# Kernel tuning notes

Hardware: AMD Instinct MI355X
Metric: run time of the kernel (lower is better)

The kernel has to match this reference:

```python
import jax, jax.numpy as jnp
import numpy as np

N_HEAD = 8
NORM_GROUPS = 32
EPS = 1e-6


def setup_inputs() -> dict:
    key = jax.random.key(0)
    ks = jax.random.split(key, 9)
    B, C, H, W, D = 1, 256, 16, 16, 16
    COND = 512
    x = jax.random.normal(ks[0], (B, C, H, W, D), dtype=jnp.float32)
    cond = jax.random.normal(ks[1], (B, COND), dtype=jnp.float32)
    # AdaGN linear scale/shift (torch Linear: weight [C, cond_dim], bias [C])
    w_scale = jax.random.normal(ks[2], (C, COND), dtype=jnp.float32) * 0.02
    b_scale = jax.random.normal(ks[3], (C,), dtype=jnp.float32) * 0.02
    w_shift = jax.random.normal(ks[4], (C, COND), dtype=jnp.float32) * 0.02
    b_shift = jax.random.normal(ks[5], (C,), dtype=jnp.float32) * 0.02
    # 1x1x1 conv3d weights collapse to matrices: qkv [3C, C] (no bias), out [C, C] + bias
    w_qkv = jax.random.normal(ks[6], (3 * C, C), dtype=jnp.float32) * (1.0 / np.sqrt(C))
    w_out = jax.random.normal(ks[7], (C, C), dtype=jnp.float32) * (1.0 / np.sqrt(C))
    b_out = jax.random.normal(ks[8], (C,), dtype=jnp.float32) * 0.02
    return {"x": x, "cond": cond, "w_scale": w_scale, "b_scale": b_scale,
            "w_shift": w_shift, "b_shift": b_shift, "w_qkv": w_qkv,
            "w_out": w_out, "b_out": b_out}


def _ada_gn(x, cond, w_scale, b_scale, w_shift, b_shift):
    B, C, H, W, D = x.shape
    G = NORM_GROUPS
    xg = x.reshape(B, G, C // G, H, W, D)
    mean = jnp.mean(xg, axis=(2, 3, 4, 5), keepdims=True)
    var = jnp.var(xg, axis=(2, 3, 4, 5), keepdims=True)
    x_norm = ((xg - mean) * jax.lax.rsqrt(var + EPS)).reshape(B, C, H, W, D)
    scale = (cond @ w_scale.T + b_scale)[:, :, None, None, None]  # [B,C,1,1,1]
    shift = (cond @ w_shift.T + b_shift)[:, :, None, None, None]
    return x_norm * (1.0 + scale) + shift


def reference(x, cond, w_scale, b_scale, w_shift, b_shift, w_qkv, w_out, b_out):
    B, C, H, W, D = x.shape
    nh = N_HEAD
    hd = C // nh
    N = H * W * D  # flattened spatial tokens
    norm = _ada_gn(x, cond, w_scale, b_scale, w_shift, b_shift)
    # 1x1x1 conv == channel matmul
    qkv = jnp.einsum('oc,bchwd->bohwd', w_qkv, norm)        # [B,3C,H,W,D]
    qkv = qkv.reshape(B, nh, 3 * hd, N)
    q, k, v = jnp.split(qkv, 3, axis=2)                      # each [B,nh,hd,N]
    attn = jnp.einsum('bnci,bncj->bnij', q, k) / jnp.sqrt(jnp.float32(C))
    attn = jax.nn.softmax(attn, axis=-1)                     # [B,nh,N,N]
    out = jnp.einsum('bnij,bncj->bnci', attn, v)             # [B,nh,hd,N]
    out = out.reshape(B, C, H, W, D)
    out = jnp.einsum('oc,bchwd->bohwd', w_out, out) + b_out[None, :, None, None, None]
    return out + x
```

## Files before the change

kernel.cpp:

```cpp
#include <hip/hip_runtime.h>
#include <math.h>

#define CCH 256
#define NN  4096
#define NHEAD 8
#define CONDD 512

typedef __attribute__((ext_vector_type(8))) short short8;
typedef __attribute__((ext_vector_type(4))) float f32x4;
typedef __attribute__((ext_vector_type(16))) float f32x16;

static __device__ __forceinline__ short f2bf(float f) {
    union { float f; uint32_t u; } v; v.f = f;
    uint32_t r = v.u + 0x7fffu + ((v.u >> 16) & 1u);
    return (short)(r >> 16);
}

static __device__ __forceinline__ uint32_t cvt_pk_bf16(float a, float b) {
    uint32_t r;
    asm("v_cvt_pk_bf16_f32 %0, %1, %2" : "=v"(r) : "v"(a), "v"(b));
    return r;
}

__global__ __launch_bounds__(256) void front_fused(const float* __restrict__ x,
                                                   const float* __restrict__ cond,
                                                   const float* __restrict__ w_scale,
                                                   const float* __restrict__ b_scale,
                                                   const float* __restrict__ w_shift,
                                                   const float* __restrict__ b_shift,
                                                   const float* __restrict__ wq,
                                                   const float* __restrict__ wo,
                                                   float* __restrict__ partial,
                                                   float* __restrict__ scale,
                                                   float* __restrict__ shift,
                                                   short* __restrict__ wqb,
                                                   short* __restrict__ wob) {
    __shared__ float rs[4], rss[4];
    int bb = blockIdx.x;
    int t = threadIdx.x;
    if (bb < 256) {
        const float4* p = (const float4*)(x + bb * 4096);
        float s = 0.f, ss = 0.f;
        for (int k = t; k < 1024; k += 256) {
            float4 v = p[k];
            s += v.x + v.y + v.z + v.w;
            ss += v.x * v.x + v.y * v.y + v.z * v.z + v.w * v.w;
        }
        #pragma unroll
        for (int off = 32; off; off >>= 1) { s += __shfl_xor(s, off); ss += __shfl_xor(ss, off); }
        int wid = t >> 6;
        if ((t & 63) == 0) { rs[wid] = s; rss[wid] = ss; }
        __syncthreads();
        if (t == 0) {
            partial[2 * bb] = rs[0] + rs[1] + rs[2] + rs[3];
            partial[2 * bb + 1] = rss[0] + rss[1] + rss[2] + rss[3];
        }
    } else if (bb < 1280) {
        int idx = (bb - 256) * 256 + t;
        if (idx < 196608) wqb[idx] = f2bf(wq[idx]);
        else              wob[idx - 196608] = f2bf(wo[idx - 196608]);
    } else {
        int o = (bb - 1280) * 4 + (t >> 6);
        int lane = t & 63;
        float ds = 0.f, dh = 0.f;
        for (int k = lane; k < CONDD; k += 64) {
            float cv = cond[k];
            ds += cv * w_scale[o * CONDD + k];
            dh += cv * w_shift[o * CONDD + k];
        }
        #pragma unroll
        for (int off = 32; off; off >>= 1) { ds += __shfl_xor(ds, off); dh += __shfl_xor(dh, off); }
        if (lane == 0) { scale[o] = ds + b_scale[o]; shift[o] = dh + b_shift[o]; }
    }
}

__global__ __launch_bounds__(256) void normalize_t(const float* __restrict__ x,
                                                   const float* __restrict__ partial,
                                                   const float* __restrict__ scale,
                                                   const float* __restrict__ shift,
                                                   short* __restrict__ norm_t) {
    __shared__ float gm[8], gr[8];
    __shared__ float Aa[64], Bb[64];
    __shared__ short tile[32 * 66];
    int i0 = blockIdx.x * 32;
    int c0 = blockIdx.y * 64;
    int g0 = c0 >> 3;
    int t = threadIdx.x;
    if (t < 8) {
        float s = 0.f, ss = 0.f;
        #pragma unroll
        for (int ch = 0; ch < 8; ++ch) {
            s += partial[((g0 + t) * 8 + ch) * 2];
            ss += partial[((g0 + t) * 8 + ch) * 2 + 1];
        }
        float mean = s * (1.0f / 32768.0f);
        float var = ss * (1.0f / 32768.0f) - mean * mean;
        gm[t] = mean;
        gr[t] = rsqrtf(var + 1e-6f);
    }
    __syncthreads();
    if (t < 64) {
        int c = c0 + t;
        float a = gr[t >> 3] * (1.0f + scale[c]);
        Aa[t] = a;
        Bb[t] = shift[c] - gm[t >> 3] * a;
    }
    __syncthreads();
    #pragma unroll
    for (int e0 = 0; e0 < 8; ++e0) {
        int e = e0 * 256 + t;
        int cl = e >> 5, il = e & 31;
        float v = x[(c0 + cl) * NN + i0 + il];
        tile[il * 66 + cl] = f2bf(v * Aa[cl] + Bb[cl]);
    }
    __syncthreads();
    #pragma unroll
    for (int e0 = 0; e0 < 4; ++e0) {
        int e = e0 * 256 + t;
        int il = e >> 5, cd = e & 31;
        uint32_t d = *(const uint32_t*)&tile[il * 66 + 2 * cd];
        *(uint32_t*)&norm_t[(i0 + il) * 256 + c0 + 2 * cd] = d;
    }
}

__global__ __launch_bounds__(256) void qkv_gemm(const short* __restrict__ wqb,
                                                const short* __restrict__ norm_t,
                                                short* __restrict__ qtb, short* __restrict__ ktb,
                                                short* __restrict__ vcb) {
    int t = threadIdx.x;
    int w = t >> 6, lane = t & 63, li = lane & 15, lg = lane >> 4;
    int o0 = blockIdx.x * 32;
    int i0 = blockIdx.y * 64 + w * 16;
    f32x4 acc[2] = {{0,0,0,0},{0,0,0,0}};
    const short* bbase = norm_t + (i0 + li) * 256 + 8 * lg;
    const short* abase = wqb + (o0 + li) * 256 + 8 * lg;
    #pragma unroll
    for (int ks = 0; ks < 8; ++ks) {
        short8 bfrag = *(const short8*)(bbase + ks * 32);
        #pragma unroll
        for (int f = 0; f < 2; ++f) {
            short8 afrag = *(const short8*)(abase + f * 16 * 256 + ks * 32);
            acc[f] = __builtin_amdgcn_mfma_f32_16x16x32_bf16(afrag, bfrag, acc[f], 0, 0, 0);
        }
    }
    int i = i0 + li;
    #pragma unroll
    for (int f = 0; f < 2; ++f) {
        #pragma unroll
        for (int r = 0; r < 4; ++r) {
            int o = o0 + 16 * f + 4 * lg + r;
            float v = acc[f][r];
            int h = o / 96;
            int rr = o - h * 96;
            int cc = rr & 31;
            int kind = rr >> 5;
            if (kind == 0)      qtb[(h * NN + i) * 32 + cc] = f2bf(v * (0.0625f * 1.44269504f));
            else if (kind == 1) ktb[(h * NN + i) * 32 + cc] = f2bf(v);
            else                vcb[(h * 32 + cc) * NN + i] = f2bf(v);
        }
    }
}

__global__ __launch_bounds__(512, 4) void attention_mfma(const short* __restrict__ qtb,
                                                         const short* __restrict__ ktb,
                                                         const short* __restrict__ vcb,
                                                         float* __restrict__ pacc,
                                                         float* __restrict__ plsum) {
    __shared__ __align__(16) char lds[49152];

    int bid = blockIdx.x;
    int h = bid & 7;
    int qb = (bid >> 3) & 15;
    int kh = bid >> 7;
    int t = threadIdx.x;
    int w = t >> 6, lane = t & 63, l31 = lane & 31, hi = lane >> 5;

    int qbase = qb * 256 + w * 32;
    const short* qrow = qtb + (h * NN + qbase + l31) * 32;
    short8 qf0 = *(const short8*)(qrow + 8 * hi);
    short8 qf1 = *(const short8*)(qrow + 16 + 8 * hi);
    asm volatile("s_waitcnt vmcnt(0)" ::: "memory");

    const char* src0;
    const char* src1;
    int ldsoff0, ldsoff1, step;
    if (w < 4) {
        int row_l = lane >> 2, g_lds = lane & 3;
        int g_glob = g_lds ^ (row_l & 3);
        const char* kbase = (const char*)ktb + (size_t)(h * NN + kh * 1024) * 64;
        int s0 = 2 * w, s1 = 2 * w + 1;
        src0 = kbase + ((s0 >> 2) * 64 + (s0 & 3) * 16 + row_l) * 64 + g_glob * 16;
        src1 = kbase + ((s1 >> 2) * 64 + (s1 & 3) * 16 + row_l) * 64 + g_glob * 16;
        ldsoff0 = s0 * 1024;
        ldsoff1 = s1 * 1024;
        step = 8192;
    } else {
        int row_l = lane >> 3, vs_lds = lane & 7;
        int vg = vs_lds ^ row_l;
        const char* vbase = (const char*)vcb + (size_t)(h * 32) * (NN * 2) + kh * 2048;
        int s0 = 2 * (w - 4), s1 = 2 * (w - 4) + 1;
        src0 = vbase + (size_t)((s0 & 3) * 8 + row_l) * (NN * 2) + (s0 >> 2) * 128 + vg * 16;
        src1 = vbase + (size_t)((s1 & 3) * 8 + row_l) * (NN * 2) + (s1 >> 2) * 128 + vg * 16;
        ldsoff0 = 8192 + s0 * 1024;
        ldsoff1 = 8192 + s1 * 1024;
        step = 256;
    }

    f32x16 acc = {0,0,0,0,0,0,0,0,0,0,0,0,0,0,0,0};
    const f32x16 zero16 = {0,0,0,0,0,0,0,0,0,0,0,0,0,0,0,0};
    float lsum = 0.f;

    #define ISSUE(st, b) do { \
        __builtin_amdgcn_global_load_lds((const uint32_t*)(src0 + (st) * step), \
            (uint32_t*)(lds + (b) * 16384 + ldsoff0), 16, 0, 0); \
        __builtin_amdgcn_global_load_lds((const uint32_t*)(src1 + (st) * step), \
            (uint32_t*)(lds + (b) * 16384 + ldsoff1), 16, 0, 0); \
    } while (0)

    #define COMPUTE(b) do { \
        const char* bb_ = lds + (b) * 16384; \
        _Pragma("unroll") \
        for (int chunk = 0; chunk < 2; ++chunk) { \
            _Pragma("unroll") \
            for (int half = 0; half < 2; ++half) { \
                int jl = half * 32; \
                int R = jl + l31; \
                int rx = R & 3; \
                const char* kr = bb_ + chunk * 4096 + R * 64; \
                short8 kf0 = *(const short8*)(kr + (((hi) ^ rx) << 4)); \
                short8 kf1 = *(const short8*)(kr + (((2 + hi) ^ rx) << 4)); \
                const char* vr = bb_ + 8192 + chunk * 4096 + l31 * 128; \
                int cx = l31 & 7; \
                int sv = (jl >> 3) + hi; \
                short8 vf0 = *(const short8*)(vr + ((sv ^ cx) << 4)); \
                short8 vf1 = *(const short8*)(vr + (((sv + 2) ^ cx) << 4)); \
                __builtin_amdgcn_s_setprio(1); \
                f32x16 s = __builtin_amdgcn_mfma_f32_32x32x16_bf16(kf0, qf0, zero16, 0, 0, 0); \
                s = __builtin_amdgcn_mfma_f32_32x32x16_bf16(kf1, qf1, s, 0, 0, 0); \
                __builtin_amdgcn_s_setprio(0); \
                float p[16]; \
                _Pragma("unroll") \
                for (int r = 0; r < 16; ++r) p[r] = __builtin_amdgcn_exp2f(s[r]); \
                float u0 = 0.f, u1 = 0.f; \
                _Pragma("unroll") \
                for (int r = 0; r < 4; ++r) { u0 += p[r] + p[4 + r]; u1 += p[8 + r] + p[12 + r]; } \
                lsum += u0 + u1; \
                auto A1 = __builtin_amdgcn_permlane32_swap(cvt_pk_bf16(p[0], p[1]),   cvt_pk_bf16(p[4], p[5]),   false, false); \
                auto A2 = __builtin_amdgcn_permlane32_swap(cvt_pk_bf16(p[2], p[3]),   cvt_pk_bf16(p[6], p[7]),   false, false); \
                auto A3 = __builtin_amdgcn_permlane32_swap(cvt_pk_bf16(p[8], p[9]),   cvt_pk_bf16(p[12], p[13]), false, false); \
                auto A4 = __builtin_amdgcn_permlane32_swap(cvt_pk_bf16(p[10], p[11]), cvt_pk_bf16(p[14], p[15]), false, false); \
                union PF { uint32_t u[4]; short8 s8; }; \
                PF f1, f2; \
                f1.u[0] = A1[0]; f1.u[1] = A2[0]; f1.u[2] = A1[1]; f1.u[3] = A2[1]; \
                f2.u[0] = A3[0]; f2.u[1] = A4[0]; f2.u[2] = A3[1]; f2.u[3] = A4[1]; \
                __builtin_amdgcn_s_setprio(1); \
                acc = __builtin_amdgcn_mfma_f32_32x32x16_bf16(vf0, f1.s8, acc, 0, 0, 0); \
                acc = __builtin_amdgcn_mfma_f32_32x32x16_bf16(vf1, f2.s8, acc, 0, 0, 0); \
                __builtin_amdgcn_s_setprio(0); \
            } \
        } \
    } while (0)

    ISSUE(0, 0);
    ISSUE(1, 1);
    ISSUE(2, 2);
    asm volatile("s_waitcnt vmcnt(4)" ::: "memory");
    __builtin_amdgcn_s_barrier();

    #pragma unroll
    for (int st = 0; st < 5; ++st) {
        COMPUTE(st % 3);
        __builtin_amdgcn_s_barrier();
        ISSUE(st + 3, st % 3);
        asm volatile("s_waitcnt vmcnt(4)" ::: "memory");
        __builtin_amdgcn_s_barrier();
    }
    COMPUTE(2);
    __builtin_amdgcn_s_barrier();
    asm volatile("s_waitcnt vmcnt(2)" ::: "memory");
    __builtin_amdgcn_s_barrier();
    COMPUTE(0);
    __builtin_amdgcn_s_barrier();
    asm volatile("s_waitcnt vmcnt(0)" ::: "memory");
    __builtin_amdgcn_s_barrier();
    COMPUTE(1);

    #undef ISSUE
    #undef COMPUTE

    lsum += __shfl_xor(lsum, 32);

    int qg = qbase + l31;
    float* pb = pacc + ((kh * 8 + h) * 32) * NN + qg;
    #pragma unroll
    for (int r = 0; r < 16; ++r) {
        int c = (r & 3) + 8 * (r >> 2) + 4 * hi;
        pb[c * NN] = acc[r];
    }
    if (hi == 0) plsum[(kh * 8 + h) * NN + qg] = lsum;
}

__global__ __launch_bounds__(256) void attn_merge(const float* __restrict__ pacc,
                                                  const float* __restrict__ plsum,
                                                  short* __restrict__ attnT) {
    __shared__ float tile[64][33];
    __shared__ float invl[64];
    int it = blockIdx.x;
    int h = blockIdx.y;
    int t = threadIdx.x;
    int i0 = it * 64;
    int c = t >> 3, ic = (t & 7) * 8;
    const float* p0 = pacc + (h * 32 + c) * NN + i0 + ic;
    #pragma unroll
    for (int k = 0; k < 8; ++k) {
        float s = 0.f;
        #pragma unroll
        for (int q4 = 0; q4 < 4; ++q4) s += p0[q4 * 8 * 32 * NN + k];
        tile[ic + k][c] = s;
    }
    if (t < 64) {
        float ls = 0.f;
        #pragma unroll
        for (int q4 = 0; q4 < 4; ++q4) ls += plsum[(q4 * 8 + h) * NN + i0 + t];
        invl[t] = 1.0f / ls;
    }
    __syncthreads();
    int i = t >> 2, cs = (t & 3) * 8;
    float iv = invl[i];
    const float* tr = &tile[i][cs];
    uint4 o;
    o.x = cvt_pk_bf16(tr[0] * iv, tr[1] * iv);
    o.y = cvt_pk_bf16(tr[2] * iv, tr[3] * iv);
    o.z = cvt_pk_bf16(tr[4] * iv, tr[5] * iv);
    o.w = cvt_pk_bf16(tr[6] * iv, tr[7] * iv);
    *(uint4*)&attnT[(i0 + i) * 256 + h * 32 + cs] = o;
}

__global__ __launch_bounds__(256) void proj_gemm(const short* __restrict__ wob,
                                                 const short* __restrict__ attnT,
                                                 const float* __restrict__ b_out,
                                                 const float* __restrict__ x,
                                                 float* __restrict__ out) {
    int t = threadIdx.x;
    int w = t >> 6, lane = t & 63, li = lane & 15, lg = lane >> 4;
    int o0 = blockIdx.x * 32;
    int i0 = blockIdx.y * 64 + w * 16;
    f32x4 acc[2] = {{0,0,0,0},{0,0,0,0}};
    const short* bbase = attnT + (i0 + li) * 256 + 8 * lg;
    const short* abase = wob + (o0 + li) * 256 + 8 * lg;
    #pragma unroll
    for (int ks = 0; ks < 8; ++ks) {
        short8 bfrag = *(const short8*)(bbase + ks * 32);
        #pragma unroll
        for (int f = 0; f < 2; ++f) {
            short8 afrag = *(const short8*)(abase + f * 16 * 256 + ks * 32);
            acc[f] = __builtin_amdgcn_mfma_f32_16x16x32_bf16(afrag, bfrag, acc[f], 0, 0, 0);
        }
    }
    int i = i0 + li;
    #pragma unroll
    for (int f = 0; f < 2; ++f) {
        #pragma unroll
        for (int r = 0; r < 4; ++r) {
            int o = o0 + 16 * f + 4 * lg + r;
            out[o * NN + i] = acc[f][r] + b_out[o] + x[o * NN + i];
        }
    }
}

extern "C" void kernel_launch(void* const* d_in, const int* in_sizes, int n_in,
                              void* d_out, int out_size, void* d_ws, size_t ws_size,
                              hipStream_t stream) {
    const float* x       = (const float*)d_in[0];
    const float* cond    = (const float*)d_in[1];
    const float* w_scale = (const float*)d_in[2];
    const float* b_scale = (const float*)d_in[3];
    const float* w_shift = (const float*)d_in[4];
    const float* b_shift = (const float*)d_in[5];
    const float* w_qkv   = (const float*)d_in[6];
    const float* w_out   = (const float*)d_in[7];
    const float* b_out   = (const float*)d_in[8];
    float* out = (float*)d_out;

    float* ws = (float*)d_ws;
    float* scale   = ws;
    float* shift   = ws + 256;
    float* partial = ws + 512;
    short* norm_t = (short*)(ws + 1024);
    short* qtb = norm_t + 1048576;
    short* ktb = qtb + 1048576;
    short* vcb = ktb + 1048576;
    short* attnT = vcb + 1048576;
    short* wqb = attnT + 1048576;
    short* wob = wqb + 768 * 256;
    float* pacc  = (float*)(wob + 65536);
    float* plsum = pacc + 4 * 8 * 32 * NN;

    front_fused<<<1344, 256, 0, stream>>>(x, cond, w_scale, b_scale, w_shift, b_shift,
                                          w_qkv, w_out, partial, scale, shift, wqb, wob);
    normalize_t<<<dim3(128, 4), 256, 0, stream>>>(x, partial, scale, shift, norm_t);
    qkv_gemm<<<dim3(24, 64), 256, 0, stream>>>(wqb, norm_t, qtb, ktb, vcb);
    attention_mfma<<<512, 512, 0, stream>>>(qtb, ktb, vcb, pacc, plsum);
    attn_merge<<<dim3(64, 8), 256, 0, stream>>>(pacc, plsum, attnT);
    proj_gemm<<<dim3(8, 64), 256, 0, stream>>>(wob, attnT, b_out, x, out);
}
```

Measured before the change: 70.54 us.

## Split attention into smaller blocks with eight key-splits and halved LDS stages

Attention blocks shrink from 512 to 256 threads, covering 128 queries instead of 256 and splitting the keys eight ways instead of four, for 2048 blocks. Each pipeline stage now loads 64 keys into 8 KB of LDS, so more blocks fit per CU and the GPU's compute units get more even work. In exchange the partial accumulators double in size and the merge kernel reads eight partials per output, which adds memory traffic. Index arithmetic is widened to size_t for the larger partial buffer.

```diff
diff --git a/kernel.cpp b/kernel.cpp
--- a/kernel.cpp
+++ b/kernel.cpp
@@ -161,103 +161,82 @@
     }
 }
 
-__global__ __launch_bounds__(512, 4) void attention_mfma(const short* __restrict__ qtb,
+__global__ __launch_bounds__(256, 6) void attention_mfma(const short* __restrict__ qtb,
                                                          const short* __restrict__ ktb,
                                                          const short* __restrict__ vcb,
                                                          float* __restrict__ pacc,
                                                          float* __restrict__ plsum) {
-    __shared__ __align__(16) char lds[49152];
+    __shared__ __align__(16) char lds[24576];
 
     int bid = blockIdx.x;
     int h = bid & 7;
-    int qb = (bid >> 3) & 15;
-    int kh = bid >> 7;
+    int qb = (bid >> 3) & 31;
+    int kh = bid >> 8;
     int t = threadIdx.x;
     int w = t >> 6, lane = t & 63, l31 = lane & 31, hi = lane >> 5;
 
-    int qbase = qb * 256 + w * 32;
+    int qbase = qb * 128 + w * 32;
     const short* qrow = qtb + (h * NN + qbase + l31) * 32;
     short8 qf0 = *(const short8*)(qrow + 8 * hi);
     short8 qf1 = *(const short8*)(qrow + 16 + 8 * hi);
     asm volatile("s_waitcnt vmcnt(0)" ::: "memory");
 
-    const char* src0;
-    const char* src1;
-    int ldsoff0, ldsoff1, step;
-    if (w < 4) {
-        int row_l = lane >> 2, g_lds = lane & 3;
-        int g_glob = g_lds ^ (row_l & 3);
-        const char* kbase = (const char*)ktb + (size_t)(h * NN + kh * 1024) * 64;
-        int s0 = 2 * w, s1 = 2 * w + 1;
-        src0 = kbase + ((s0 >> 2) * 64 + (s0 & 3) * 16 + row_l) * 64 + g_glob * 16;
-        src1 = kbase + ((s1 >> 2) * 64 + (s1 & 3) * 16 + row_l) * 64 + g_glob * 16;
-        ldsoff0 = s0 * 1024;
-        ldsoff1 = s1 * 1024;
-        step = 8192;
-    } else {
-        int row_l = lane >> 3, vs_lds = lane & 7;
-        int vg = vs_lds ^ row_l;
-        const char* vbase = (const char*)vcb + (size_t)(h * 32) * (NN * 2) + kh * 2048;
-        int s0 = 2 * (w - 4), s1 = 2 * (w - 4) + 1;
-        src0 = vbase + (size_t)((s0 & 3) * 8 + row_l) * (NN * 2) + (s0 >> 2) * 128 + vg * 16;
-        src1 = vbase + (size_t)((s1 & 3) * 8 + row_l) * (NN * 2) + (s1 >> 2) * 128 + vg * 16;
-        ldsoff0 = 8192 + s0 * 1024;
-        ldsoff1 = 8192 + s1 * 1024;
-        step = 256;
-    }
+    int kr_ = t >> 2, ks_ = t & 3, kg_ = ks_ ^ (kr_ & 3);
+    int vr_ = t >> 3, vs_ = t & 7, vg_ = vs_ ^ (vr_ & 7);
+    const char* ksrc = (const char*)(ktb + (size_t)(h * NN + kh * 512) * 32) + kr_ * 64 + kg_ * 16;
+    const char* vsrc = (const char*)(vcb + (size_t)(h * 32 + vr_) * NN + kh * 512) + vg_ * 16;
+    int koff = w * 1024;
+    int voff = 4096 + w * 1024;
 
     f32x16 acc = {0,0,0,0,0,0,0,0,0,0,0,0,0,0,0,0};
     const f32x16 zero16 = {0,0,0,0,0,0,0,0,0,0,0,0,0,0,0,0};
     float lsum = 0.f;
 
     #define ISSUE(st, b) do { \
-        __builtin_amdgcn_global_load_lds((const uint32_t*)(src0 + (st) * step), \
-            (uint32_t*)(lds + (b) * 16384 + ldsoff0), 16, 0, 0); \
-        __builtin_amdgcn_global_load_lds((const uint32_t*)(src1 + (st) * step), \
-            (uint32_t*)(lds + (b) * 16384 + ldsoff1), 16, 0, 0); \
+        __builtin_amdgcn_global_load_lds((const uint32_t*)(ksrc + (st) * 4096), \
+            (uint32_t*)(lds + (b) * 8192 + koff), 16, 0, 0); \
+        __builtin_amdgcn_global_load_lds((const uint32_t*)(vsrc + (st) * 128), \
+            (uint32_t*)(lds + (b) * 8192 + voff), 16, 0, 0); \
     } while (0)
 
     #define COMPUTE(b) do { \
-        const char* bb_ = lds + (b) * 16384; \
+        const char* bb_ = lds + (b) * 8192; \
         _Pragma("unroll") \
-        for (int chunk = 0; chunk < 2; ++chunk) { \
+        for (int half = 0; half < 2; ++half) { \
+            int jl = half * 32; \
+            int R = jl + l31; \
+            int rx = R & 3; \
+            const char* kr = bb_ + R * 64; \
+            short8 kf0 = *(const short8*)(kr + (((hi) ^ rx) << 4)); \
+            short8 kf1 = *(const short8*)(kr + (((2 + hi) ^ rx) << 4)); \
+            const char* vr = bb_ + 4096 + l31 * 128; \
+            int cx = l31 & 7; \
+            int sv = (jl >> 3) + hi; \
+            short8 vf0 = *(const short8*)(vr + ((sv ^ cx) << 4)); \
+            short8 vf1 = *(const short8*)(vr + (((sv + 2) ^ cx) << 4)); \
+            __builtin_amdgcn_s_setprio(1); \
+            f32x16 s = __builtin_amdgcn_mfma_f32_32x32x16_bf16(kf0, qf0, zero16, 0, 0, 0); \
+            s = __builtin_amdgcn_mfma_f32_32x32x16_bf16(kf1, qf1, s, 0, 0, 0); \
+            __builtin_amdgcn_s_setprio(0); \
+            float p[16]; \
             _Pragma("unroll") \
-            for (int half = 0; half < 2; ++half) { \
-                int jl = half * 32; \
-                int R = jl + l31; \
-                int rx = R & 3; \
-                const char* kr = bb_ + chunk * 4096 + R * 64; \
-                short8 kf0 = *(const short8*)(kr + (((hi) ^ rx) << 4)); \
-                short8 kf1 = *(const short8*)(kr + (((2 + hi) ^ rx) << 4)); \
-                const char* vr = bb_ + 8192 + chunk * 4096 + l31 * 128; \
-                int cx = l31 & 7; \
-                int sv = (jl >> 3) + hi; \
-                short8 vf0 = *(const short8*)(vr + ((sv ^ cx) << 4)); \
-                short8 vf1 = *(const short8*)(vr + (((sv + 2) ^ cx) << 4)); \
-                __builtin_amdgcn_s_setprio(1); \
-                f32x16 s = __builtin_amdgcn_mfma_f32_32x32x16_bf16(kf0, qf0, zero16, 0, 0, 0); \
-                s = __builtin_amdgcn_mfma_f32_32x32x16_bf16(kf1, qf1, s, 0, 0, 0); \
-                __builtin_amdgcn_s_setprio(0); \
-                float p[16]; \
-                _Pragma("unroll") \
-                for (int r = 0; r < 16; ++r) p[r] = __builtin_amdgcn_exp2f(s[r]); \
-                float u0 = 0.f, u1 = 0.f; \
-                _Pragma("unroll") \
-                for (int r = 0; r < 4; ++r) { u0 += p[r] + p[4 + r]; u1 += p[8 + r] + p[12 + r]; } \
-                lsum += u0 + u1; \
-                auto A1 = __builtin_amdgcn_permlane32_swap(cvt_pk_bf16(p[0], p[1]),   cvt_pk_bf16(p[4], p[5]),   false, false); \
-                auto A2 = __builtin_amdgcn_permlane32_swap(cvt_pk_bf16(p[2], p[3]),   cvt_pk_bf16(p[6], p[7]),   false, false); \
-                auto A3 = __builtin_amdgcn_permlane32_swap(cvt_pk_bf16(p[8], p[9]),   cvt_pk_bf16(p[12], p[13]), false, false); \
-                auto A4 = __builtin_amdgcn_permlane32_swap(cvt_pk_bf16(p[10], p[11]), cvt_pk_bf16(p[14], p[15]), false, false); \
-                union PF { uint32_t u[4]; short8 s8; }; \
-                PF f1, f2; \
-                f1.u[0] = A1[0]; f1.u[1] = A2[0]; f1.u[2] = A1[1]; f1.u[3] = A2[1]; \
-                f2.u[0] = A3[0]; f2.u[1] = A4[0]; f2.u[2] = A3[1]; f2.u[3] = A4[1]; \
-                __builtin_amdgcn_s_setprio(1); \
-                acc = __builtin_amdgcn_mfma_f32_32x32x16_bf16(vf0, f1.s8, acc, 0, 0, 0); \
-                acc = __builtin_amdgcn_mfma_f32_32x32x16_bf16(vf1, f2.s8, acc, 0, 0, 0); \
-                __builtin_amdgcn_s_setprio(0); \
-            } \
+            for (int r = 0; r < 16; ++r) p[r] = __builtin_amdgcn_exp2f(s[r]); \
+            float u0 = 0.f, u1 = 0.f; \
+            _Pragma("unroll") \
+            for (int r = 0; r < 4; ++r) { u0 += p[r] + p[4 + r]; u1 += p[8 + r] + p[12 + r]; } \
+            lsum += u0 + u1; \
+            auto A1 = __builtin_amdgcn_permlane32_swap(cvt_pk_bf16(p[0], p[1]),   cvt_pk_bf16(p[4], p[5]),   false, false); \
+            auto A2 = __builtin_amdgcn_permlane32_swap(cvt_pk_bf16(p[2], p[3]),   cvt_pk_bf16(p[6], p[7]),   false, false); \
+            auto A3 = __builtin_amdgcn_permlane32_swap(cvt_pk_bf16(p[8], p[9]),   cvt_pk_bf16(p[12], p[13]), false, false); \
+            auto A4 = __builtin_amdgcn_permlane32_swap(cvt_pk_bf16(p[10], p[11]), cvt_pk_bf16(p[14], p[15]), false, false); \
+            union PF { uint32_t u[4]; short8 s8; }; \
+            PF f1, f2; \
+            f1.u[0] = A1[0]; f1.u[1] = A2[0]; f1.u[2] = A1[1]; f1.u[3] = A2[1]; \
+            f2.u[0] = A3[0]; f2.u[1] = A4[0]; f2.u[2] = A3[1]; f2.u[3] = A4[1]; \
+            __builtin_amdgcn_s_setprio(1); \
+            acc = __builtin_amdgcn_mfma_f32_32x32x16_bf16(vf0, f1.s8, acc, 0, 0, 0); \
+            acc = __builtin_amdgcn_mfma_f32_32x32x16_bf16(vf1, f2.s8, acc, 0, 0, 0); \
+            __builtin_amdgcn_s_setprio(0); \
         } \
     } while (0)
 
@@ -291,7 +270,7 @@
     lsum += __shfl_xor(lsum, 32);
 
     int qg = qbase + l31;
-    float* pb = pacc + ((kh * 8 + h) * 32) * NN + qg;
+    float* pb = pacc + (size_t)((kh * 8 + h) * 32) * NN + qg;
     #pragma unroll
     for (int r = 0; r < 16; ++r) {
         int c = (r & 3) + 8 * (r >> 2) + 4 * hi;
@@ -310,18 +289,18 @@
     int t = threadIdx.x;
     int i0 = it * 64;
     int c = t >> 3, ic = (t & 7) * 8;
-    const float* p0 = pacc + (h * 32 + c) * NN + i0 + ic;
+    const float* p0 = pacc + (size_t)(h * 32 + c) * NN + i0 + ic;
     #pragma unroll
     for (int k = 0; k < 8; ++k) {
         float s = 0.f;
         #pragma unroll
-        for (int q4 = 0; q4 < 4; ++q4) s += p0[q4 * 8 * 32 * NN + k];
+        for (int q8 = 0; q8 < 8; ++q8) s += p0[(size_t)q8 * 8 * 32 * NN + k];
         tile[ic + k][c] = s;
     }
     if (t < 64) {
         float ls = 0.f;
         #pragma unroll
-        for (int q4 = 0; q4 < 4; ++q4) ls += plsum[(q4 * 8 + h) * NN + i0 + t];
+        for (int q8 = 0; q8 < 8; ++q8) ls += plsum[(size_t)(q8 * 8 + h) * NN + i0 + t];
         invl[t] = 1.0f / ls;
     }
     __syncthreads();
@@ -394,13 +373,13 @@
     short* wqb = attnT + 1048576;
     short* wob = wqb + 768 * 256;
     float* pacc  = (float*)(wob + 65536);
-    float* plsum = pacc + 4 * 8 * 32 * NN;
+    float* plsum = pacc + (size_t)8 * 8 * 32 * NN;
 
     front_fused<<<1344, 256, 0, stream>>>(x, cond, w_scale, b_scale, w_shift, b_shift,
                                           w_qkv, w_out, partial, scale, shift, wqb, wob);
     normalize_t<<<dim3(128, 4), 256, 0, stream>>>(x, partial, scale, shift, norm_t);
     qkv_gemm<<<dim3(24, 64), 256, 0, stream>>>(wqb, norm_t, qtb, ktb, vcb);
-    attention_mfma<<<512, 512, 0, stream>>>(qtb, ktb, vcb, pacc, plsum);
+    attention_mfma<<<2048, 256, 0, stream>>>(qtb, ktb, vcb, pacc, plsum);
     attn_merge<<<dim3(64, 8), 256, 0, stream>>>(pacc, plsum, attnT);
     proj_gemm<<<dim3(8, 64), 256, 0, stream>>>(wob, attnT, b_out, x, out);
 }
```

New measurement: 74.10 us. 5.0% more time.

## Fold split-KV attention merge into output projection GEMM, store partials as bf16

Applied to the files above, without the earlier changes.

Removes the attn_merge kernel. The attention kernel now writes its unnormalized per-split partial outputs as bf16, transposed through LDS into a token-major layout. The projection GEMM reads the per-head row-sum partials and computes 1/l per (head, token). It then runs MFMAs over all four key-split partials and scales each head's contribution by that inverse. This saves one launch and the fp32 partial round trip. The cost is a 4x larger K dimension in proj_gemm and extra bf16 rounding of the unnormalized partials.

```diff
diff --git a/kernel.cpp b/kernel.cpp
--- a/kernel.cpp
+++ b/kernel.cpp
@@ -164,7 +164,7 @@
 __global__ __launch_bounds__(512, 4) void attention_mfma(const short* __restrict__ qtb,
                                                          const short* __restrict__ ktb,
                                                          const short* __restrict__ vcb,
-                                                         float* __restrict__ pacc,
+                                                         short* __restrict__ attnP,
                                                          float* __restrict__ plsum) {
     __shared__ __align__(16) char lds[49152];
 
@@ -288,83 +288,80 @@
     #undef ISSUE
     #undef COMPUTE
 
+    __builtin_amdgcn_s_barrier();
+
     lsum += __shfl_xor(lsum, 32);
 
-    int qg = qbase + l31;
-    float* pb = pacc + ((kh * 8 + h) * 32) * NN + qg;
-    #pragma unroll
-    for (int r = 0; r < 16; ++r) {
-        int c = (r & 3) + 8 * (r >> 2) + 4 * hi;
-        pb[c * NN] = acc[r];
-    }
-    if (hi == 0) plsum[(kh * 8 + h) * NN + qg] = lsum;
-}
-
-__global__ __launch_bounds__(256) void attn_merge(const float* __restrict__ pacc,
-                                                  const float* __restrict__ plsum,
-                                                  short* __restrict__ attnT) {
-    __shared__ float tile[64][33];
-    __shared__ float invl[64];
-    int it = blockIdx.x;
-    int h = blockIdx.y;
-    int t = threadIdx.x;
-    int i0 = it * 64;
-    int c = t >> 3, ic = (t & 7) * 8;
-    const float* p0 = pacc + (h * 32 + c) * NN + i0 + ic;
-    #pragma unroll
-    for (int k = 0; k < 8; ++k) {
-        float s = 0.f;
-        #pragma unroll
-        for (int q4 = 0; q4 < 4; ++q4) s += p0[q4 * 8 * 32 * NN + k];
-        tile[ic + k][c] = s;
-    }
-    if (t < 64) {
-        float ls = 0.f;
-        #pragma unroll
-        for (int q4 = 0; q4 < 4; ++q4) ls += plsum[(q4 * 8 + h) * NN + i0 + t];
-        invl[t] = 1.0f / ls;
-    }
-    __syncthreads();
-    int i = t >> 2, cs = (t & 3) * 8;
-    float iv = invl[i];
-    const float* tr = &tile[i][cs];
-    uint4 o;
-    o.x = cvt_pk_bf16(tr[0] * iv, tr[1] * iv);
-    o.y = cvt_pk_bf16(tr[2] * iv, tr[3] * iv);
-    o.z = cvt_pk_bf16(tr[4] * iv, tr[5] * iv);
-    o.w = cvt_pk_bf16(tr[6] * iv, tr[7] * iv);
-    *(uint4*)&attnT[(i0 + i) * 256 + h * 32 + cs] = o;
+    short* tile = (short*)lds + w * 1024;
+    #pragma unroll
+    for (int g = 0; g < 4; ++g) {
+        uint2 u;
+        u.x = cvt_pk_bf16(acc[4 * g + 0], acc[4 * g + 1]);
+        u.y = cvt_pk_bf16(acc[4 * g + 2], acc[4 * g + 3]);
+        *(uint2*)(tile + l31 * 32 + 8 * g + 4 * hi) = u;
+    }
+    {
+        int row = l31, half = hi;
+        const uint4* srcp = (const uint4*)(tile + row * 32 + half * 16);
+        short* dst = attnP + (size_t)(qbase + row) * 1024 + kh * 256 + h * 32 + half * 16;
+        uint4 d0 = srcp[0];
+        uint4 d1 = srcp[1];
+        *(uint4*)dst = d0;
+        *(uint4*)(dst + 8) = d1;
+    }
+    if (hi == 0) plsum[(size_t)(kh * 8 + h) * NN + qbase + l31] = lsum;
 }
 
 __global__ __launch_bounds__(256) void proj_gemm(const short* __restrict__ wob,
-                                                 const short* __restrict__ attnT,
+                                                 const short* __restrict__ attnP,
+                                                 const float* __restrict__ plsum,
                                                  const float* __restrict__ b_out,
                                                  const float* __restrict__ x,
                                                  float* __restrict__ out) {
+    __shared__ float invl[8][64];
     int t = threadIdx.x;
     int w = t >> 6, lane = t & 63, li = lane & 15, lg = lane >> 4;
     int o0 = blockIdx.x * 32;
-    int i0 = blockIdx.y * 64 + w * 16;
-    f32x4 acc[2] = {{0,0,0,0},{0,0,0,0}};
-    const short* bbase = attnT + (i0 + li) * 256 + 8 * lg;
+    int i0b = blockIdx.y * 64;
+    int i0 = i0b + w * 16;
+    {
+        int hh = t >> 5, ii = (t & 31) * 2;
+        float a = 0.f, b = 0.f;
+        #pragma unroll
+        for (int kh = 0; kh < 4; ++kh) {
+            const float* pl = plsum + (size_t)(kh * 8 + hh) * NN + i0b;
+            a += pl[ii];
+            b += pl[ii + 1];
+        }
+        invl[hh][ii] = 1.0f / a;
+        invl[hh][ii + 1] = 1.0f / b;
+    }
+    __syncthreads();
+    const short* bbase = attnP + (size_t)(i0 + li) * 1024 + 8 * lg;
     const short* abase = wob + (o0 + li) * 256 + 8 * lg;
-    #pragma unroll
-    for (int ks = 0; ks < 8; ++ks) {
-        short8 bfrag = *(const short8*)(bbase + ks * 32);
-        #pragma unroll
-        for (int f = 0; f < 2; ++f) {
-            short8 afrag = *(const short8*)(abase + f * 16 * 256 + ks * 32);
-            acc[f] = __builtin_amdgcn_mfma_f32_16x16x32_bf16(afrag, bfrag, acc[f], 0, 0, 0);
-        }
+    f32x4 facc0 = {0, 0, 0, 0}, facc1 = {0, 0, 0, 0};
+    #pragma unroll
+    for (int h = 0; h < 8; ++h) {
+        short8 af0 = *(const short8*)(abase + h * 32);
+        short8 af1 = *(const short8*)(abase + 16 * 256 + h * 32);
+        f32x4 acc0 = {0, 0, 0, 0}, acc1 = {0, 0, 0, 0};
+        #pragma unroll
+        for (int kh = 0; kh < 4; ++kh) {
+            short8 bf = *(const short8*)(bbase + kh * 256 + h * 32);
+            acc0 = __builtin_amdgcn_mfma_f32_16x16x32_bf16(af0, bf, acc0, 0, 0, 0);
+            acc1 = __builtin_amdgcn_mfma_f32_16x16x32_bf16(af1, bf, acc1, 0, 0, 0);
+        }
+        float iv = invl[h][w * 16 + li];
+        facc0 += acc0 * iv;
+        facc1 += acc1 * iv;
     }
     int i = i0 + li;
     #pragma unroll
-    for (int f = 0; f < 2; ++f) {
-        #pragma unroll
-        for (int r = 0; r < 4; ++r) {
-            int o = o0 + 16 * f + 4 * lg + r;
-            out[o * NN + i] = acc[f][r] + b_out[o] + x[o * NN + i];
-        }
+    for (int r = 0; r < 4; ++r) {
+        int o = o0 + 4 * lg + r;
+        out[o * NN + i] = facc0[r] + b_out[o] + x[o * NN + i];
+        int o2 = o0 + 16 + 4 * lg + r;
+        out[o2 * NN + i] = facc1[r] + b_out[o2] + x[o2 * NN + i];
     }
 }
 
@@ -390,17 +387,15 @@
     short* qtb = norm_t + 1048576;
     short* ktb = qtb + 1048576;
     short* vcb = ktb + 1048576;
-    short* attnT = vcb + 1048576;
-    short* wqb = attnT + 1048576;
-    short* wob = wqb + 768 * 256;
-    float* pacc  = (float*)(wob + 65536);
-    float* plsum = pacc + 4 * 8 * 32 * NN;
+    short* wqb = vcb + 1048576;
+    short* wob = wqb + 196608;
+    short* attnP = wob + 65536;
+    float* plsum = (float*)(attnP + (size_t)4096 * 1024);
 
     front_fused<<<1344, 256, 0, stream>>>(x, cond, w_scale, b_scale, w_shift, b_shift,
                                           w_qkv, w_out, partial, scale, shift, wqb, wob);
     normalize_t<<<dim3(128, 4), 256, 0, stream>>>(x, partial, scale, shift, norm_t);
     qkv_gemm<<<dim3(24, 64), 256, 0, stream>>>(wqb, norm_t, qtb, ktb, vcb);
-    attention_mfma<<<512, 512, 0, stream>>>(qtb, ktb, vcb, pacc, plsum);
-    attn_merge<<<dim3(64, 8), 256, 0, stream>>>(pacc, plsum, attnT);
-    proj_gemm<<<dim3(8, 64), 256, 0, stream>>>(wob, attnT, b_out, x, out);
-}
+    attention_mfma<<<512, 512, 0, stream>>>(qtb, ktb, vcb, attnP, plsum);
+    proj_gemm<<<dim3(8, 64), 256, 0, stream>>>(wob, attnP, plsum, b_out, x, out);
+}
```

Result: slower. 73.56 us (+4.3%).

## Fuse GroupNorm apply into QKV GEMM and vectorize weight bf16 conversion

Applied to the files above, without the earlier changes.

Removes the separate normalize_t kernel and the norm_t round trip through global memory. The QKV GEMM now normalizes its own 64-token x tile into LDS and uses it as the B operand, with larger 128-output tiles per block. Weight conversion to bf16 now uses float4 loads and packed cvt, so fewer blocks are needed in front_fused. The cost is that x is re-read and re-normalized by each of the 6 output-column blocks, and the grid is much smaller, which lowers parallelism. Some index math is also widened to size_t.

```diff
diff --git a/kernel.cpp b/kernel.cpp
--- a/kernel.cpp
+++ b/kernel.cpp
@@ -55,12 +55,23 @@
             partial[2 * bb] = rs[0] + rs[1] + rs[2] + rs[3];
             partial[2 * bb + 1] = rss[0] + rss[1] + rss[2] + rss[3];
         }
-    } else if (bb < 1280) {
-        int idx = (bb - 256) * 256 + t;
-        if (idx < 196608) wqb[idx] = f2bf(wq[idx]);
-        else              wob[idx - 196608] = f2bf(wo[idx - 196608]);
+    } else if (bb < 512) {
+        int idx4 = (bb - 256) * 256 + t;
+        if (idx4 < 49152) {
+            float4 v = ((const float4*)wq)[idx4];
+            uint2 u;
+            u.x = cvt_pk_bf16(v.x, v.y);
+            u.y = cvt_pk_bf16(v.z, v.w);
+            *(uint2*)&wqb[idx4 * 4] = u;
+        } else {
+            float4 v = ((const float4*)wo)[idx4 - 49152];
+            uint2 u;
+            u.x = cvt_pk_bf16(v.x, v.y);
+            u.y = cvt_pk_bf16(v.z, v.w);
+            *(uint2*)&wob[(idx4 - 49152) * 4] = u;
+        }
     } else {
-        int o = (bb - 1280) * 4 + (t >> 6);
+        int o = (bb - 512) * 4 + (t >> 6);
         int lane = t & 63;
         float ds = 0.f, dh = 0.f;
         for (int k = lane; k < CONDD; k += 64) {
@@ -74,78 +85,73 @@
     }
 }
 
-__global__ __launch_bounds__(256) void normalize_t(const float* __restrict__ x,
-                                                   const float* __restrict__ partial,
-                                                   const float* __restrict__ scale,
-                                                   const float* __restrict__ shift,
-                                                   short* __restrict__ norm_t) {
-    __shared__ float gm[8], gr[8];
-    __shared__ float Aa[64], Bb[64];
-    __shared__ short tile[32 * 66];
-    int i0 = blockIdx.x * 32;
-    int c0 = blockIdx.y * 64;
-    int g0 = c0 >> 3;
+__global__ __launch_bounds__(256, 4) void qkv_fused(const float* __restrict__ x,
+                                                    const float* __restrict__ partial,
+                                                    const float* __restrict__ scale,
+                                                    const float* __restrict__ shift,
+                                                    const short* __restrict__ wqb,
+                                                    short* __restrict__ qtb, short* __restrict__ ktb,
+                                                    short* __restrict__ vcb) {
+    __shared__ float Af[256], Bf[256];
+    __shared__ __align__(16) short nt[16384];
+
     int t = threadIdx.x;
-    if (t < 8) {
+    int o0 = blockIdx.x * 128;
+    int i0 = blockIdx.y * 64;
+
+    {
+        int c = t;
+        int g = c >> 3;
         float s = 0.f, ss = 0.f;
         #pragma unroll
         for (int ch = 0; ch < 8; ++ch) {
-            s += partial[((g0 + t) * 8 + ch) * 2];
-            ss += partial[((g0 + t) * 8 + ch) * 2 + 1];
+            s += partial[(g * 8 + ch) * 2];
+            ss += partial[(g * 8 + ch) * 2 + 1];
         }
         float mean = s * (1.0f / 32768.0f);
         float var = ss * (1.0f / 32768.0f) - mean * mean;
-        gm[t] = mean;
-        gr[t] = rsqrtf(var + 1e-6f);
+        float rstd = rsqrtf(var + 1e-6f);
+        float a = rstd * (1.0f + scale[c]);
+        Af[c] = a;
+        Bf[c] = shift[c] - mean * a;
     }
     __syncthreads();
-    if (t < 64) {
-        int c = c0 + t;
-        float a = gr[t >> 3] * (1.0f + scale[c]);
-        Aa[t] = a;
-        Bb[t] = shift[c] - gm[t >> 3] * a;
+
+    #pragma unroll
+    for (int e = 0; e < 8; ++e) {
+        int task = e * 256 + t;
+        int il = task & 63;
+        int slot = task >> 6;
+        int c0 = slot * 8;
+        union { short s[8]; short8 v; } pk;
+        #pragma unroll
+        for (int j = 0; j < 8; ++j) {
+            float v = x[(c0 + j) * NN + i0 + il];
+            pk.s[j] = f2bf(v * Af[c0 + j] + Bf[c0 + j]);
+        }
+        *(short8*)((char*)nt + slot * 1024 + il * 16) = pk.v;
     }
     __syncthreads();
-    #pragma unroll
-    for (int e0 = 0; e0 < 8; ++e0) {
-        int e = e0 * 256 + t;
-        int cl = e >> 5, il = e & 31;
-        float v = x[(c0 + cl) * NN + i0 + il];
-        tile[il * 66 + cl] = f2bf(v * Aa[cl] + Bb[cl]);
-    }
-    __syncthreads();
-    #pragma unroll
-    for (int e0 = 0; e0 < 4; ++e0) {
-        int e = e0 * 256 + t;
-        int il = e >> 5, cd = e & 31;
-        uint32_t d = *(const uint32_t*)&tile[il * 66 + 2 * cd];
-        *(uint32_t*)&norm_t[(i0 + il) * 256 + c0 + 2 * cd] = d;
-    }
-}
-
-__global__ __launch_bounds__(256) void qkv_gemm(const short* __restrict__ wqb,
-                                                const short* __restrict__ norm_t,
-                                                short* __restrict__ qtb, short* __restrict__ ktb,
-                                                short* __restrict__ vcb) {
-    int t = threadIdx.x;
+
     int w = t >> 6, lane = t & 63, li = lane & 15, lg = lane >> 4;
-    int o0 = blockIdx.x * 32;
-    int i0 = blockIdx.y * 64 + w * 16;
-    f32x4 acc[2] = {{0,0,0,0},{0,0,0,0}};
-    const short* bbase = norm_t + (i0 + li) * 256 + 8 * lg;
+    int irow = w * 16 + li;
+
+    f32x4 acc[8] = {{0,0,0,0},{0,0,0,0},{0,0,0,0},{0,0,0,0},
+                    {0,0,0,0},{0,0,0,0},{0,0,0,0},{0,0,0,0}};
     const short* abase = wqb + (o0 + li) * 256 + 8 * lg;
     #pragma unroll
     for (int ks = 0; ks < 8; ++ks) {
-        short8 bfrag = *(const short8*)(bbase + ks * 32);
-        #pragma unroll
-        for (int f = 0; f < 2; ++f) {
+        int slot = ks * 4 + lg;
+        short8 bfrag = *(const short8*)((char*)nt + slot * 1024 + irow * 16);
+        #pragma unroll
+        for (int f = 0; f < 8; ++f) {
             short8 afrag = *(const short8*)(abase + f * 16 * 256 + ks * 32);
             acc[f] = __builtin_amdgcn_mfma_f32_16x16x32_bf16(afrag, bfrag, acc[f], 0, 0, 0);
         }
     }
-    int i = i0 + li;
-    #pragma unroll
-    for (int f = 0; f < 2; ++f) {
+    int i = i0 + irow;
+    #pragma unroll
+    for (int f = 0; f < 8; ++f) {
         #pragma unroll
         for (int r = 0; r < 4; ++r) {
             int o = o0 + 16 * f + 4 * lg + r;
@@ -291,13 +297,13 @@
     lsum += __shfl_xor(lsum, 32);
 
     int qg = qbase + l31;
-    float* pb = pacc + ((kh * 8 + h) * 32) * NN + qg;
+    float* pb = pacc + (size_t)((kh * 8 + h) * 32) * NN + qg;
     #pragma unroll
     for (int r = 0; r < 16; ++r) {
         int c = (r & 3) + 8 * (r >> 2) + 4 * hi;
         pb[c * NN] = acc[r];
     }
-    if (hi == 0) plsum[(kh * 8 + h) * NN + qg] = lsum;
+    if (hi == 0) plsum[(size_t)(kh * 8 + h) * NN + qg] = lsum;
 }
 
 __global__ __launch_bounds__(256) void attn_merge(const float* __restrict__ pacc,
@@ -310,18 +316,18 @@
     int t = threadIdx.x;
     int i0 = it * 64;
     int c = t >> 3, ic = (t & 7) * 8;
-    const float* p0 = pacc + (h * 32 + c) * NN + i0 + ic;
+    const float* p0 = pacc + (size_t)(h * 32 + c) * NN + i0 + ic;
     #pragma unroll
     for (int k = 0; k < 8; ++k) {
         float s = 0.f;
         #pragma unroll
-        for (int q4 = 0; q4 < 4; ++q4) s += p0[q4 * 8 * 32 * NN + k];
+        for (int q4 = 0; q4 < 4; ++q4) s += p0[(size_t)q4 * 8 * 32 * NN + k];
         tile[ic + k][c] = s;
     }
     if (t < 64) {
         float ls = 0.f;
         #pragma unroll
-        for (int q4 = 0; q4 < 4; ++q4) ls += plsum[(q4 * 8 + h) * NN + i0 + t];
+        for (int q4 = 0; q4 < 4; ++q4) ls += plsum[(size_t)(q4 * 8 + h) * NN + i0 + t];
         invl[t] = 1.0f / ls;
     }
     __syncthreads();
@@ -386,20 +392,18 @@
     float* scale   = ws;
     float* shift   = ws + 256;
     float* partial = ws + 512;
-    short* norm_t = (short*)(ws + 1024);
-    short* qtb = norm_t + 1048576;
+    short* qtb = (short*)(ws + 1024);
     short* ktb = qtb + 1048576;
     short* vcb = ktb + 1048576;
     short* attnT = vcb + 1048576;
     short* wqb = attnT + 1048576;
-    short* wob = wqb + 768 * 256;
+    short* wob = wqb + 196608;
     float* pacc  = (float*)(wob + 65536);
-    float* plsum = pacc + 4 * 8 * 32 * NN;
-
-    front_fused<<<1344, 256, 0, stream>>>(x, cond, w_scale, b_scale, w_shift, b_shift,
-                                          w_qkv, w_out, partial, scale, shift, wqb, wob);
-    normalize_t<<<dim3(128, 4), 256, 0, stream>>>(x, partial, scale, shift, norm_t);
-    qkv_gemm<<<dim3(24, 64), 256, 0, stream>>>(wqb, norm_t, qtb, ktb, vcb);
+    float* plsum = pacc + (size_t)4 * 8 * 32 * NN;
+
+    front_fused<<<576, 256, 0, stream>>>(x, cond, w_scale, b_scale, w_shift, b_shift,
+                                         w_qkv, w_out, partial, scale, shift, wqb, wob);
+    qkv_fused<<<dim3(6, 64), 256, 0, stream>>>(x, partial, scale, shift, wqb, qtb, ktb, vcb);
     attention_mfma<<<512, 512, 0, stream>>>(qtb, ktb, vcb, pacc, plsum);
     attn_merge<<<dim3(64, 8), 256, 0, stream>>>(pacc, plsum, attnT);
     proj_gemm<<<dim3(8, 64), 256, 0, stream>>>(wob, attnT, b_out, x, out);
```

Result: slower. 72.05 us (+2.1%).
